# Optimization experiments

Hardware: AMD Instinct MI355X
Metric: run time of the kernel (lower is better)

The kernel has to match this reference:

```python
import jax, jax.numpy as jnp
import numpy as np

N = 16384          # num nodes
D = 128            # feature dim
STRENGTH = 0.1     # connection_strength
K = min(10, N // 10)  # = 10, per original code
EPS = 1e-12        # F.normalize eps


def setup_inputs() -> dict:
    key = jax.random.key(0)
    k1, k2, k3 = jax.random.split(key, 3)
    feat = jax.random.normal(k1, (N, D), jnp.float32)
    # Linear(dim, dim, bias=False) weight, xavier_normal_ gain=1.0 -> std = sqrt(2/(D+D))
    W = jax.random.normal(k2, (D, D), jnp.float32) * np.sqrt(2.0 / (D + D)).astype(np.float32)
    # meta_path_embedding [1, D], xavier_normal_ gain=0.1
    emb = jax.random.normal(k3, (1, D), jnp.float32) * (0.1 * np.sqrt(2.0 / (1 + D))).astype(np.float32)
    return {"feat": feat, "W": W, "emb": emb}


def reference(feat, W, emb):
    # projected_feat = Linear(feat) ; torch Linear: x @ W.T
    proj = feat @ W.T                                   # [N, D]
    # L2-normalize rows (torch F.normalize, eps=1e-12)
    nrm = proj / jnp.maximum(jnp.linalg.norm(proj, axis=1, keepdims=True), EPS)
    sims = nrm @ nrm.T                                  # [N, N]
    # top-(k+1) neighbors per row (self usually included since sim=1)
    vals, idx = jax.lax.top_k(sims, K + 1)              # [N, K+1]
    rows = jnp.arange(N)[:, None]
    mask = idx != rows                                  # drop self-edges
    # per-row softmax over valid (non-self) topk values == torch per-row F.softmax loop
    masked = jnp.where(mask, vals, -jnp.inf)
    w = jax.nn.softmax(masked, axis=1)
    w = jnp.where(mask, w, 0.0)                         # [N, K+1]
    # sparse propagation: propagated[r] = sum_j w[r,j] * proj[idx[r,j]]
    gathered = proj[idx]                                # [N, K+1, D]
    propagated = jnp.einsum('nk,nkd->nd', w, gathered)  # [N, D]
    meta_signal = STRENGTH * (propagated + emb)
    return feat + meta_signal
```

## Files before the change

### kernel.cpp

```cpp
#include <hip/hip_runtime.h>
#include <hip/hip_bf16.h>

#define NN 16384
#define DD 128
#define KP1 11
#define NSPLIT 8
#define CBLK 32
#define COLS_PER_SPLIT (NN / NSPLIT)
#define NITER (COLS_PER_SPLIT / CBLK)

typedef __attribute__((ext_vector_type(8))) short bf16x8;
typedef __attribute__((ext_vector_type(4))) float f32x4;
typedef __attribute__((ext_vector_type(16))) float f32x16;
typedef unsigned int u32;

__global__ __launch_bounds__(256) void phaseA_kernel(
    const float* __restrict__ feat, const float* __restrict__ W,
    float* __restrict__ proj, __hip_bfloat16* __restrict__ nrmb) {
  __shared__ float Wl[DD][132];
  __shared__ float fl[16][DD];
  const int t = threadIdx.x;
  const int blk = blockIdx.x;

  const f32x4* W4 = (const f32x4*)W;
#pragma unroll
  for (int i = 0; i < 16; ++i) {
    int f4 = t + 256 * i;
    *(f32x4*)&Wl[f4 >> 5][(f4 & 31) * 4] = W4[f4];
  }
  const f32x4* F4 = (const f32x4*)(feat + (size_t)blk * 16 * DD);
#pragma unroll
  for (int i = 0; i < 2; ++i) {
    int f4 = t + 256 * i;
    *(f32x4*)&fl[f4 >> 5][(f4 & 31) * 4] = F4[f4];
  }
  __syncthreads();

  const int w = t >> 6, l = t & 63;
#pragma unroll 1
  for (int q = 0; q < 4; ++q) {
    const int rloc = w * 4 + q;
    const int r = blk * 16 + rloc;
    float a0 = 0.f, a1 = 0.f;
#pragma unroll
    for (int k = 0; k < DD; k += 4) {
      f32x4 fv = *(const f32x4*)&fl[rloc][k];
      f32x4 w0 = *(const f32x4*)&Wl[l][k];
      f32x4 w1 = *(const f32x4*)&Wl[l + 64][k];
      a0 += fv[0] * w0[0] + fv[1] * w0[1] + fv[2] * w0[2] + fv[3] * w0[3];
      a1 += fv[0] * w1[0] + fv[1] * w1[1] + fv[2] * w1[2] + fv[3] * w1[3];
    }
    float n2 = a0 * a0 + a1 * a1;
#pragma unroll
    for (int o = 32; o > 0; o >>= 1) n2 += __shfl_xor(n2, o);
    float invn = 1.0f / fmaxf(sqrtf(n2), 1e-12f);
    proj[(size_t)r * DD + l] = a0;
    proj[(size_t)r * DD + l + 64] = a1;
    nrmb[(size_t)r * DD + l] = __float2bfloat16(a0 * invn);
    nrmb[(size_t)r * DD + l + 64] = __float2bfloat16(a1 * invn);
  }
}

#define LADDM(CKE)                                                         \
  { u32 ck = (CKE);                                                        \
    u32 n0 = k0 > ck ? k0 : ck;                                            \
    u32 n1, n2, n3, n4, n5, n6, n7, n8, n9, n10;                           \
    asm("v_med3_u32 %0,%1,%2,%3" : "=v"(n1) : "v"(ck), "v"(k1), "v"(k0));  \
    asm("v_med3_u32 %0,%1,%2,%3" : "=v"(n2) : "v"(ck), "v"(k2), "v"(k1));  \
    asm("v_med3_u32 %0,%1,%2,%3" : "=v"(n3) : "v"(ck), "v"(k3), "v"(k2));  \
    asm("v_med3_u32 %0,%1,%2,%3" : "=v"(n4) : "v"(ck), "v"(k4), "v"(k3));  \
    asm("v_med3_u32 %0,%1,%2,%3" : "=v"(n5) : "v"(ck), "v"(k5), "v"(k4));  \
    asm("v_med3_u32 %0,%1,%2,%3" : "=v"(n6) : "v"(ck), "v"(k6), "v"(k5));  \
    asm("v_med3_u32 %0,%1,%2,%3" : "=v"(n7) : "v"(ck), "v"(k7), "v"(k6));  \
    asm("v_med3_u32 %0,%1,%2,%3" : "=v"(n8) : "v"(ck), "v"(k8), "v"(k7));  \
    asm("v_med3_u32 %0,%1,%2,%3" : "=v"(n9) : "v"(ck), "v"(k9), "v"(k8));  \
    asm("v_med3_u32 %0,%1,%2,%3" : "=v"(n10) : "v"(ck), "v"(k10), "v"(k9));\
    k0 = n0; k1 = n1; k2 = n2; k3 = n3; k4 = n4; k5 = n5;                  \
    k6 = n6; k7 = n7; k8 = n8; k9 = n9; k10 = n10; }

#define INS1(vv, off)                                                      \
  LADDM(((__float_as_uint((vv) + 2.0f) & 0xFFFFF800u) |                    \
         (u32)(loid - (off))))

#define SCAN16(ACC, TBASE)                                                 \
  { const int loid = 2047 - (TBASE) - 4 * hi;                              \
    INS1(ACC[0], 0)   INS1(ACC[1], 1)   INS1(ACC[2], 2)                    \
    INS1(ACC[3], 3)   INS1(ACC[4], 8)   INS1(ACC[5], 9)                    \
    INS1(ACC[6], 10)  INS1(ACC[7], 11)  INS1(ACC[8], 16)                   \
    INS1(ACC[9], 17)  INS1(ACC[10], 18) INS1(ACC[11], 19)                  \
    INS1(ACC[12], 24) INS1(ACC[13], 25) INS1(ACC[14], 26)                  \
    INS1(ACC[15], 27) }

#define GRAM(ACC, P)                                                       \
  { _Pragma("unroll")                                                      \
    for (int i_ = 0; i_ < 16; ++i_) ACC[i_] = 0.f;                         \
    const char* cb_ = (const char*)&cand[P][0];                            \
    __builtin_amdgcn_s_setprio(1);                                         \
    _Pragma("unroll")                                                      \
    for (int kt = 0; kt < 8; ++kt) {                                       \
      bf16x8 cv = *(const bf16x8*)(cb_ + dso[kt]);                         \
      ACC = __builtin_amdgcn_mfma_f32_32x32x16_bf16(cv, rowF[kt], ACC,     \
                                                    0, 0, 0);              \
    }                                                                      \
    __builtin_amdgcn_s_setprio(0); }

__device__ __forceinline__ void gload_lds16(const void* g, void* l) {
  __builtin_amdgcn_global_load_lds(
      (const __attribute__((address_space(1))) unsigned int*)g,
      (__attribute__((address_space(3))) unsigned int*)l, 16, 0, 0);
}

__global__ __launch_bounds__(256, 4) void phaseB_kernel(
    const __hip_bfloat16* __restrict__ nrmb, u32* __restrict__ tk) {
  __shared__ __hip_bfloat16 cand[2][CBLK * DD];
  const int t = threadIdx.x;
  const int w = t >> 6, l = t & 63;
  const int l31 = l & 31, hi = l >> 5;
  const int rb = blockIdx.x >> 3;
  const int cs = blockIdx.x & 7;
  const int r0 = rb * 128 + w * 32;
  const int csbase = cs * COLS_PER_SPLIT;
  const unsigned short* nb = (const unsigned short*)nrmb;

  bf16x8 rowF[8];
#pragma unroll
  for (int kt = 0; kt < 8; ++kt)
    rowF[kt] = *(const bf16x8*)(nb + (size_t)(r0 + l31) * DD + kt * 16 + hi * 8);

  const int swsalt = (l31 & 7);
  int dso[8];
#pragma unroll
  for (int kt = 0; kt < 8; ++kt)
    dso[kt] = l31 * 256 + (((kt * 2 + hi) ^ swsalt) << 4);

  u32 k0 = 0, k1 = 0, k2 = 0, k3 = 0, k4 = 0, k5 = 0,
      k6 = 0, k7 = 0, k8 = 0, k9 = 0, k10 = 0;

#define STAGE(bufidx, itile)                                                  \
  {                                                                           \
    const unsigned short* srcb = nb + (size_t)(csbase + (itile)*CBLK) * DD;   \
    _Pragma("unroll")                                                         \
    for (int j = 0; j < 2; ++j) {                                             \
      int cl = w * 8 + j * 4 + (l >> 4);                                      \
      int ch = (l & 15) ^ (cl & 7);                                           \
      gload_lds16(srcb + (size_t)cl * DD + ch * 8,                            \
                  &cand[bufidx][w * 1024 + j * 512]);                         \
    }                                                                         \
  }

  STAGE(0, 0);
  __syncthreads();

  f32x16 aA, aB;
#pragma unroll 1
  for (int tt = 0; tt < NITER / 2; ++tt) {
    const int t0 = 2 * tt;
    if (t0 + 1 < NITER) STAGE(1, t0 + 1);
    GRAM(aA, 0)
    if (tt > 0) { SCAN16(aB, (t0 - 1) * CBLK) }
    __syncthreads();
    if (t0 + 2 < NITER) STAGE(0, t0 + 2);
    GRAM(aB, 1)
    SCAN16(aA, t0 * CBLK)
    __syncthreads();
  }
  SCAN16(aB, (NITER - 1) * CBLK)

  {
    int m0 = __shfl_xor((int)k0, 32);
    int m1 = __shfl_xor((int)k1, 32);
    int m2 = __shfl_xor((int)k2, 32);
    int m3 = __shfl_xor((int)k3, 32);
    int m4 = __shfl_xor((int)k4, 32);
    int m5 = __shfl_xor((int)k5, 32);
    int m6 = __shfl_xor((int)k6, 32);
    int m7 = __shfl_xor((int)k7, 32);
    int m8 = __shfl_xor((int)k8, 32);
    int m9 = __shfl_xor((int)k9, 32);
    int m10 = __shfl_xor((int)k10, 32);
    LADDM((u32)m0)
    LADDM((u32)m1)
    LADDM((u32)m2)
    LADDM((u32)m3)
    LADDM((u32)m4)
    LADDM((u32)m5)
    LADDM((u32)m6)
    LADDM((u32)m7)
    LADDM((u32)m8)
    LADDM((u32)m9)
    LADDM((u32)m10)
  }

  if (hi == 0) {
    const int myr = r0 + l31;
    u32* ov = tk + ((size_t)cs * NN + myr) * KP1;
    ov[0] = k0; ov[1] = k1; ov[2] = k2; ov[3] = k3; ov[4] = k4; ov[5] = k5;
    ov[6] = k6; ov[7] = k7; ov[8] = k8; ov[9] = k9; ov[10] = k10;
  }
#undef STAGE
}

__global__ __launch_bounds__(256) void phaseC_kernel(
    const float* __restrict__ proj, const float* __restrict__ feat,
    const float* __restrict__ emb, const u32* __restrict__ tk,
    float* __restrict__ out) {
  const int t = threadIdx.x, w = t >> 6, l = t & 63;
  const int r = blockIdx.x * 4 + w;

  float v0, v1 = -3.0e38f;
  int i0, i1 = 0x7fffffff;
  {
    int j = l, s = j / KP1, k = j - s * KP1;
    u32 key = tk[((size_t)s * NN + r) * KP1 + k];
    v0 = __uint_as_float(key & 0xFFFFF800u) - 2.0f;
    i0 = (s << 11) + 2047 - (int)(key & 2047u);
  }
  if (l < 88 - 64) {
    int j = 64 + l, s = j / KP1, k = j - s * KP1;
    u32 key = tk[((size_t)s * NN + r) * KP1 + k];
    v1 = __uint_as_float(key & 0xFFFFF800u) - 2.0f;
    i1 = (s << 11) + 2047 - (int)(key & 2047u);
  }

  bool t0 = false, t1 = false;
  float selv[KP1]; int seli[KP1];
#pragma unroll
  for (int s = 0; s < KP1; ++s) {
    float bv = -3.0e38f; int bi = 0x7fffffff;
    if (!t0 && (v0 > bv || (v0 == bv && i0 < bi))) { bv = v0; bi = i0; }
    if (!t1 && (v1 > bv || (v1 == bv && i1 < bi))) { bv = v1; bi = i1; }
#pragma unroll
    for (int o = 32; o > 0; o >>= 1) {
      float ovv = __shfl_xor(bv, o);
      int obi = __shfl_xor(bi, o);
      if (ovv > bv || (ovv == bv && obi < bi)) { bv = ovv; bi = obi; }
    }
    selv[s] = bv; seli[s] = bi;
    if (!t0 && i0 == bi) t0 = true;
    else if (!t1 && i1 == bi) t1 = true;
  }

  float m = -3.0e38f;
#pragma unroll
  for (int s = 0; s < KP1; ++s)
    if (seli[s] != r) m = fmaxf(m, selv[s]);
  float den = 0.f; float wg[KP1];
#pragma unroll
  for (int s = 0; s < KP1; ++s) {
    float e = (seli[s] != r) ? __expf(selv[s] - m) : 0.f;
    wg[s] = e; den += e;
  }
  const float rden = 1.0f / den;

  float p0 = 0.f, p1 = 0.f;
#pragma unroll
  for (int s = 0; s < KP1; ++s) {
    const float* pr = proj + (size_t)seli[s] * DD;
    float ws = wg[s] * rden;
    p0 += ws * pr[l];
    p1 += ws * pr[l + 64];
  }
  out[(size_t)r * DD + l] = feat[(size_t)r * DD + l] + 0.1f * (p0 + emb[l]);
  out[(size_t)r * DD + l + 64] =
      feat[(size_t)r * DD + l + 64] + 0.1f * (p1 + emb[l + 64]);
}

extern "C" void kernel_launch(void* const* d_in, const int* in_sizes, int n_in,
                              void* d_out, int out_size, void* d_ws, size_t ws_size,
                              hipStream_t stream) {
  (void)in_sizes; (void)n_in; (void)out_size; (void)ws_size;
  const float* feat = (const float*)d_in[0];
  const float* W    = (const float*)d_in[1];
  const float* emb  = (const float*)d_in[2];
  float* out = (float*)d_out;

  char* ws = (char*)d_ws;
  float* proj          = (float*)ws;
  __hip_bfloat16* nrmb = (__hip_bfloat16*)(ws + (size_t)NN * DD * 4);
  u32* tk = (u32*)(ws + (size_t)NN * DD * 6);

  phaseA_kernel<<<NN / 16, 256, 0, stream>>>(feat, W, proj, nrmb);
  phaseB_kernel<<<128 * NSPLIT, 256, 0, stream>>>(nrmb, tk);
  phaseC_kernel<<<NN / 4, 256, 0, stream>>>(proj, feat, emb, tk, out);
}
```

Baseline: 203.6 us.

## Load candidate tiles directly into registers and use single-wave blocks in phaseB

Drops the LDS double-buffered staging of candidate column tiles in the similarity/top-k kernel. Each wave now loads its candidate fragments straight from global memory into registers, prefetching the next tile while it scans the current one. Blocks shrink to one wave and the grid grows by four. This removes LDS traffic and block-wide barriers, but candidate tiles are no longer shared across the four waves, so L2/global reads rise about fourfold and load latency is less hidden.

```diff
diff --git a/kernel.cpp b/kernel.cpp
--- a/kernel.cpp
+++ b/kernel.cpp
@@ -91,34 +91,14 @@
     INS1(ACC[12], 24) INS1(ACC[13], 25) INS1(ACC[14], 26)                  \
     INS1(ACC[15], 27) }
 
-#define GRAM(ACC, P)                                                       \
-  { _Pragma("unroll")                                                      \
-    for (int i_ = 0; i_ < 16; ++i_) ACC[i_] = 0.f;                         \
-    const char* cb_ = (const char*)&cand[P][0];                            \
-    __builtin_amdgcn_s_setprio(1);                                         \
-    _Pragma("unroll")                                                      \
-    for (int kt = 0; kt < 8; ++kt) {                                       \
-      bf16x8 cv = *(const bf16x8*)(cb_ + dso[kt]);                         \
-      ACC = __builtin_amdgcn_mfma_f32_32x32x16_bf16(cv, rowF[kt], ACC,     \
-                                                    0, 0, 0);              \
-    }                                                                      \
-    __builtin_amdgcn_s_setprio(0); }
-
-__device__ __forceinline__ void gload_lds16(const void* g, void* l) {
-  __builtin_amdgcn_global_load_lds(
-      (const __attribute__((address_space(1))) unsigned int*)g,
-      (__attribute__((address_space(3))) unsigned int*)l, 16, 0, 0);
-}
-
-__global__ __launch_bounds__(256, 4) void phaseB_kernel(
+__global__ __launch_bounds__(64, 4) void phaseB_kernel(
     const __hip_bfloat16* __restrict__ nrmb, u32* __restrict__ tk) {
-  __shared__ __hip_bfloat16 cand[2][CBLK * DD];
-  const int t = threadIdx.x;
-  const int w = t >> 6, l = t & 63;
+  const int l = threadIdx.x;
   const int l31 = l & 31, hi = l >> 5;
-  const int rb = blockIdx.x >> 3;
-  const int cs = blockIdx.x & 7;
-  const int r0 = rb * 128 + w * 32;
+  const int gb = blockIdx.x;
+  const int cs = gb & 7;
+  const int rg = gb >> 3;
+  const int r0 = rg * 32;
   const int csbase = cs * COLS_PER_SPLIT;
   const unsigned short* nb = (const unsigned short*)nrmb;
 
@@ -127,44 +107,35 @@
   for (int kt = 0; kt < 8; ++kt)
     rowF[kt] = *(const bf16x8*)(nb + (size_t)(r0 + l31) * DD + kt * 16 + hi * 8);
 
-  const int swsalt = (l31 & 7);
-  int dso[8];
-#pragma unroll
-  for (int kt = 0; kt < 8; ++kt)
-    dso[kt] = l31 * 256 + (((kt * 2 + hi) ^ swsalt) << 4);
-
   u32 k0 = 0, k1 = 0, k2 = 0, k3 = 0, k4 = 0, k5 = 0,
       k6 = 0, k7 = 0, k8 = 0, k9 = 0, k10 = 0;
 
-#define STAGE(bufidx, itile)                                                  \
-  {                                                                           \
-    const unsigned short* srcb = nb + (size_t)(csbase + (itile)*CBLK) * DD;   \
-    _Pragma("unroll")                                                         \
-    for (int j = 0; j < 2; ++j) {                                             \
-      int cl = w * 8 + j * 4 + (l >> 4);                                      \
-      int ch = (l & 15) ^ (cl & 7);                                           \
-      gload_lds16(srcb + (size_t)cl * DD + ch * 8,                            \
-                  &cand[bufidx][w * 1024 + j * 512]);                         \
-    }                                                                         \
-  }
-
-  STAGE(0, 0);
-  __syncthreads();
-
-  f32x16 aA, aB;
+  const unsigned short* cp = nb + (size_t)(csbase + l31) * DD + hi * 8;
+
+  bf16x8 cf[8];
+#pragma unroll
+  for (int kt = 0; kt < 8; ++kt)
+    cf[kt] = *(const bf16x8*)(cp + kt * 16);
+
 #pragma unroll 1
-  for (int tt = 0; tt < NITER / 2; ++tt) {
-    const int t0 = 2 * tt;
-    if (t0 + 1 < NITER) STAGE(1, t0 + 1);
-    GRAM(aA, 0)
-    if (tt > 0) { SCAN16(aB, (t0 - 1) * CBLK) }
-    __syncthreads();
-    if (t0 + 2 < NITER) STAGE(0, t0 + 2);
-    GRAM(aB, 1)
-    SCAN16(aA, t0 * CBLK)
-    __syncthreads();
-  }
-  SCAN16(aB, (NITER - 1) * CBLK)
+  for (int t = 0; t < NITER; ++t) {
+    f32x16 acc;
+#pragma unroll
+    for (int i = 0; i < 16; ++i) acc[i] = 0.f;
+    __builtin_amdgcn_s_setprio(1);
+#pragma unroll
+    for (int kt = 0; kt < 8; ++kt)
+      acc = __builtin_amdgcn_mfma_f32_32x32x16_bf16(cf[kt], rowF[kt], acc,
+                                                    0, 0, 0);
+    __builtin_amdgcn_s_setprio(0);
+    if (t + 1 < NITER) {
+      const unsigned short* cpn = cp + (size_t)(t + 1) * CBLK * DD;
+#pragma unroll
+      for (int kt = 0; kt < 8; ++kt)
+        cf[kt] = *(const bf16x8*)(cpn + kt * 16);
+    }
+    SCAN16(acc, t * CBLK)
+  }
 
   {
     int m0 = __shfl_xor((int)k0, 32);
@@ -197,7 +168,6 @@
     ov[0] = k0; ov[1] = k1; ov[2] = k2; ov[3] = k3; ov[4] = k4; ov[5] = k5;
     ov[6] = k6; ov[7] = k7; ov[8] = k8; ov[9] = k9; ov[10] = k10;
   }
-#undef STAGE
 }
 
 __global__ __launch_bounds__(256) void phaseC_kernel(
@@ -280,6 +250,6 @@
   u32* tk = (u32*)(ws + (size_t)NN * DD * 6);
 
   phaseA_kernel<<<NN / 16, 256, 0, stream>>>(feat, W, proj, nrmb);
-  phaseB_kernel<<<128 * NSPLIT, 256, 0, stream>>>(nrmb, tk);
+  phaseB_kernel<<<512 * NSPLIT, 64, 0, stream>>>(nrmb, tk);
   phaseC_kernel<<<NN / 4, 256, 0, stream>>>(proj, feat, emb, tk, out);
 }
```

After: 306.9 us. +50.8%, slower.

## Switch similarity GEMM to 16x16x32 MFMA tiles with 16-row waves

Applied to the files above, without the earlier changes.

Restructures the top-k similarity kernel to use 16x16x32 bf16 MFMA instead of 32x32x16. Each wave now owns 16 rows, the grid doubles, and occupancy hints rise to 8 blocks per CU. The 2.0 bias is folded into the accumulator init, and the top-k merge across lanes becomes a two-step xor-shuffle over the 4 lane groups. The aim is fewer registers and more in-flight waves, overlapping MFMA with the serial median-insert scan. The cost is that each wave reloads candidate tiles for only 16 rows, so operand reuse per LDS read drops and loads rise.

```diff
diff --git a/kernel.cpp b/kernel.cpp
--- a/kernel.cpp
+++ b/kernel.cpp
@@ -5,13 +5,11 @@
 #define DD 128
 #define KP1 11
 #define NSPLIT 8
-#define CBLK 32
 #define COLS_PER_SPLIT (NN / NSPLIT)
-#define NITER (COLS_PER_SPLIT / CBLK)
+#define NPAIR 64
 
 typedef __attribute__((ext_vector_type(8))) short bf16x8;
 typedef __attribute__((ext_vector_type(4))) float f32x4;
-typedef __attribute__((ext_vector_type(16))) float f32x16;
 typedef unsigned int u32;
 
 __global__ __launch_bounds__(256) void phaseA_kernel(
@@ -79,30 +77,24 @@
     k6 = n6; k7 = n7; k8 = n8; k9 = n9; k10 = n10; }
 
 #define INS1(vv, off)                                                      \
-  LADDM(((__float_as_uint((vv) + 2.0f) & 0xFFFFF800u) |                    \
-         (u32)(loid - (off))))
-
-#define SCAN16(ACC, TBASE)                                                 \
-  { const int loid = 2047 - (TBASE) - 4 * hi;                              \
-    INS1(ACC[0], 0)   INS1(ACC[1], 1)   INS1(ACC[2], 2)                    \
-    INS1(ACC[3], 3)   INS1(ACC[4], 8)   INS1(ACC[5], 9)                    \
-    INS1(ACC[6], 10)  INS1(ACC[7], 11)  INS1(ACC[8], 16)                   \
-    INS1(ACC[9], 17)  INS1(ACC[10], 18) INS1(ACC[11], 19)                  \
-    INS1(ACC[12], 24) INS1(ACC[13], 25) INS1(ACC[14], 26)                  \
-    INS1(ACC[15], 27) }
-
-#define GRAM(ACC, P)                                                       \
-  { _Pragma("unroll")                                                      \
-    for (int i_ = 0; i_ < 16; ++i_) ACC[i_] = 0.f;                         \
-    const char* cb_ = (const char*)&cand[P][0];                            \
+  LADDM(((__float_as_uint(vv) & 0xFFFFF800u) | (u32)(loid - (off))))
+
+#define DOTILE(CBP, tp, T)                                                 \
+  { const char* cb_ = (CBP) + (T) * 4096;                                  \
+    f32x4 acc;                                                             \
+    acc[0] = 2.0f; acc[1] = 2.0f; acc[2] = 2.0f; acc[3] = 2.0f;            \
     __builtin_amdgcn_s_setprio(1);                                         \
-    _Pragma("unroll")                                                      \
-    for (int kt = 0; kt < 8; ++kt) {                                       \
-      bf16x8 cv = *(const bf16x8*)(cb_ + dso[kt]);                         \
-      ACC = __builtin_amdgcn_mfma_f32_32x32x16_bf16(cv, rowF[kt], ACC,     \
-                                                    0, 0, 0);              \
-    }                                                                      \
-    __builtin_amdgcn_s_setprio(0); }
+    acc = __builtin_amdgcn_mfma_f32_16x16x32_bf16(                         \
+        *(const bf16x8*)(cb_ + dso[0]), rowF[0], acc, 0, 0, 0);            \
+    acc = __builtin_amdgcn_mfma_f32_16x16x32_bf16(                         \
+        *(const bf16x8*)(cb_ + dso[1]), rowF[1], acc, 0, 0, 0);            \
+    acc = __builtin_amdgcn_mfma_f32_16x16x32_bf16(                         \
+        *(const bf16x8*)(cb_ + dso[2]), rowF[2], acc, 0, 0, 0);            \
+    acc = __builtin_amdgcn_mfma_f32_16x16x32_bf16(                         \
+        *(const bf16x8*)(cb_ + dso[3]), rowF[3], acc, 0, 0, 0);            \
+    __builtin_amdgcn_s_setprio(0);                                         \
+    const int loid = 2047 - ((tp) * 32 + (T) * 16) - lh * 4;               \
+    INS1(acc[0], 0) INS1(acc[1], 1) INS1(acc[2], 2) INS1(acc[3], 3) }
 
 __device__ __forceinline__ void gload_lds16(const void* g, void* l) {
   __builtin_amdgcn_global_load_lds(
@@ -110,74 +102,67 @@
       (__attribute__((address_space(3))) unsigned int*)l, 16, 0, 0);
 }
 
-__global__ __launch_bounds__(256, 4) void phaseB_kernel(
+__global__ __launch_bounds__(256, 8) void phaseB_kernel(
     const __hip_bfloat16* __restrict__ nrmb, u32* __restrict__ tk) {
-  __shared__ __hip_bfloat16 cand[2][CBLK * DD];
+  __shared__ __align__(16) char candB[2][8192];
   const int t = threadIdx.x;
   const int w = t >> 6, l = t & 63;
-  const int l31 = l & 31, hi = l >> 5;
+  const int r16i = l & 15, lh = l >> 4;
   const int rb = blockIdx.x >> 3;
   const int cs = blockIdx.x & 7;
-  const int r0 = rb * 128 + w * 32;
+  const int gr = rb * 64 + w * 16 + r16i;
   const int csbase = cs * COLS_PER_SPLIT;
   const unsigned short* nb = (const unsigned short*)nrmb;
 
-  bf16x8 rowF[8];
-#pragma unroll
-  for (int kt = 0; kt < 8; ++kt)
-    rowF[kt] = *(const bf16x8*)(nb + (size_t)(r0 + l31) * DD + kt * 16 + hi * 8);
-
-  const int swsalt = (l31 & 7);
-  int dso[8];
-#pragma unroll
-  for (int kt = 0; kt < 8; ++kt)
-    dso[kt] = l31 * 256 + (((kt * 2 + hi) ^ swsalt) << 4);
+  bf16x8 rowF[4];
+#pragma unroll
+  for (int ks = 0; ks < 4; ++ks)
+    rowF[ks] = *(const bf16x8*)(nb + (size_t)gr * DD + ks * 32 + lh * 8);
+
+  int dso[4];
+#pragma unroll
+  for (int ks = 0; ks < 4; ++ks)
+    dso[ks] = r16i * 256 + (((ks * 4 + lh) ^ (r16i & 7)) << 4);
+
+  const int loffE = lh * 256 + ((r16i ^ lh) << 4);
 
   u32 k0 = 0, k1 = 0, k2 = 0, k3 = 0, k4 = 0, k5 = 0,
       k6 = 0, k7 = 0, k8 = 0, k9 = 0, k10 = 0;
 
-#define STAGE(bufidx, itile)                                                  \
+#define STAGE(BI, tp)                                                         \
   {                                                                           \
-    const unsigned short* srcb = nb + (size_t)(csbase + (itile)*CBLK) * DD;   \
-    _Pragma("unroll")                                                         \
-    for (int j = 0; j < 2; ++j) {                                             \
-      int cl = w * 8 + j * 4 + (l >> 4);                                      \
-      int ch = (l & 15) ^ (cl & 7);                                           \
-      gload_lds16(srcb + (size_t)cl * DD + ch * 8,                            \
-                  &cand[bufidx][w * 1024 + j * 512]);                         \
-    }                                                                         \
+    const char* sb = (const char*)nb +                                        \
+                     ((size_t)(csbase + (tp) * 32) << 8) + w * 2048;          \
+    gload_lds16(sb + loffE, &candB[BI][w * 2048]);                            \
+    gload_lds16(sb + 1024 + (loffE ^ 64), &candB[BI][w * 2048 + 1024]);       \
   }
 
   STAGE(0, 0);
   __syncthreads();
 
-  f32x16 aA, aB;
 #pragma unroll 1
-  for (int tt = 0; tt < NITER / 2; ++tt) {
-    const int t0 = 2 * tt;
-    if (t0 + 1 < NITER) STAGE(1, t0 + 1);
-    GRAM(aA, 0)
-    if (tt > 0) { SCAN16(aB, (t0 - 1) * CBLK) }
+  for (int tp = 0; tp < NPAIR; ++tp) {
+    const int bi = tp & 1;
+    if (tp + 1 < NPAIR) STAGE(bi ^ 1, tp + 1);
+    const char* cbp = &candB[bi][0];
+    DOTILE(cbp, tp, 0)
+    DOTILE(cbp, tp, 1)
     __syncthreads();
-    if (t0 + 2 < NITER) STAGE(0, t0 + 2);
-    GRAM(aB, 1)
-    SCAN16(aA, t0 * CBLK)
-    __syncthreads();
-  }
-  SCAN16(aB, (NITER - 1) * CBLK)
-
-  {
-    int m0 = __shfl_xor((int)k0, 32);
-    int m1 = __shfl_xor((int)k1, 32);
-    int m2 = __shfl_xor((int)k2, 32);
-    int m3 = __shfl_xor((int)k3, 32);
-    int m4 = __shfl_xor((int)k4, 32);
-    int m5 = __shfl_xor((int)k5, 32);
-    int m6 = __shfl_xor((int)k6, 32);
-    int m7 = __shfl_xor((int)k7, 32);
-    int m8 = __shfl_xor((int)k8, 32);
-    int m9 = __shfl_xor((int)k9, 32);
-    int m10 = __shfl_xor((int)k10, 32);
+  }
+
+#pragma unroll
+  for (int d = 16; d <= 32; d <<= 1) {
+    int m0 = __shfl_xor((int)k0, d);
+    int m1 = __shfl_xor((int)k1, d);
+    int m2 = __shfl_xor((int)k2, d);
+    int m3 = __shfl_xor((int)k3, d);
+    int m4 = __shfl_xor((int)k4, d);
+    int m5 = __shfl_xor((int)k5, d);
+    int m6 = __shfl_xor((int)k6, d);
+    int m7 = __shfl_xor((int)k7, d);
+    int m8 = __shfl_xor((int)k8, d);
+    int m9 = __shfl_xor((int)k9, d);
+    int m10 = __shfl_xor((int)k10, d);
     LADDM((u32)m0)
     LADDM((u32)m1)
     LADDM((u32)m2)
@@ -191,9 +176,8 @@
     LADDM((u32)m10)
   }
 
-  if (hi == 0) {
-    const int myr = r0 + l31;
-    u32* ov = tk + ((size_t)cs * NN + myr) * KP1;
+  if (lh == 0) {
+    u32* ov = tk + ((size_t)cs * NN + gr) * KP1;
     ov[0] = k0; ov[1] = k1; ov[2] = k2; ov[3] = k3; ov[4] = k4; ov[5] = k5;
     ov[6] = k6; ov[7] = k7; ov[8] = k8; ov[9] = k9; ov[10] = k10;
   }
@@ -280,6 +264,6 @@
   u32* tk = (u32*)(ws + (size_t)NN * DD * 6);
 
   phaseA_kernel<<<NN / 16, 256, 0, stream>>>(feat, W, proj, nrmb);
-  phaseB_kernel<<<128 * NSPLIT, 256, 0, stream>>>(nrmb, tk);
+  phaseB_kernel<<<256 * NSPLIT, 256, 0, stream>>>(nrmb, tk);
   phaseC_kernel<<<NN / 4, 256, 0, stream>>>(proj, feat, emb, tk, out);
 }
```

New measurement: 214.5 us. 1.05x slower.
